# Kernel optimization log

Measured on AMD Instinct MI355X. Metric: run time of the kernel, lower is better.

## Reference

```python
import jax, jax.numpy as jnp
import numpy as np

B, S, D, H = 4, 2048, 1024, 16
HD = D // H
BITS = 8
LEVELS = 2 ** BITS - 1          # number of negative log2 levels
SCALING = 32.0 / 16.0           # lora alpha / rank for 8-bit adapter
NEG_INF = -1e9


def log_fake_quant(x, reduce_axes):
    """Per-channel log-domain fake quantization with straight-through estimator.
    Scale = per-channel max-abs; magnitudes snapped to power-of-two fractions of scale."""
    s = jnp.maximum(jnp.max(jnp.abs(x), axis=reduce_axes, keepdims=True), 1e-8)
    ratio = jnp.clip(jnp.abs(x) / s, 2.0 ** (-LEVELS), 1.0)
    e = jnp.round(jnp.log2(ratio))                      # in [-LEVELS, 0]
    q = jnp.sign(x) * s * jnp.exp2(e)
    return x + jax.lax.stop_gradient(q - x)             # STE


def cpt_linear(x, W, b, lA, lB):
    """CPTLinear: fake-quantized activation/weight GEMM + bias + LoRA on the fp input."""
    xq = log_fake_quant(x, tuple(range(x.ndim - 1)))     # per last-dim channel
    Wq = log_fake_quant(W, (1,))                         # per output row (channel_dim=0)
    out = xq @ Wq.T + b
    return out + (x @ lA @ lB) * SCALING


def setup_inputs() -> dict:
    key = jax.random.key(0)
    ks = jax.random.split(key, 8)
    causal = jnp.tril(jnp.ones((S, S), dtype=bool))
    mask = jnp.where(causal, 0.0, NEG_INF).astype(jnp.float32)[None, None]  # [1,1,S,S]
    return {
        "hidden_states": jax.random.normal(ks[0], (B, S, D), jnp.float32),
        "attention_mask": mask,
        "W_attn": jax.random.normal(ks[1], (3 * D, D), jnp.float32) * 0.02,
        "b_attn": jnp.zeros((3 * D,), jnp.float32),
        "lA_attn": jax.random.normal(ks[2], (D, 16), jnp.float32) * 0.01,
        "lB_attn": jax.random.normal(ks[3], (16, 3 * D), jnp.float32) * 0.01,
        "W_proj": jax.random.normal(ks[4], (D, D), jnp.float32) * 0.02,
        "b_proj": jnp.zeros((D,), jnp.float32),
        "lA_proj": jax.random.normal(ks[5], (D, 16), jnp.float32) * 0.01,
        "lB_proj": jax.random.normal(ks[6], (16, D), jnp.float32) * 0.01,
    }


def reference(hidden_states, attention_mask, W_attn, b_attn, lA_attn, lB_attn,
              W_proj, b_proj, lA_proj, lB_proj):
    qkv = cpt_linear(hidden_states, W_attn, b_attn, lA_attn, lB_attn)  # [B,S,3D]
    q, k, v = jnp.split(qkv, 3, axis=-1)

    def to_heads(t):
        return t.reshape(B, S, H, HD).transpose(0, 2, 1, 3)            # [B,H,S,HD]

    q, k, v = to_heads(q), to_heads(k), to_heads(v)
    scores = jnp.einsum("bhqd,bhkd->bhqk", q, k) / np.float32(np.sqrt(HD))
    scores = scores + attention_mask
    attn = jax.nn.softmax(scores, axis=-1)                             # dropout: eval mode (identity)
    out = jnp.einsum("bhqk,bhkd->bhqd", attn, v)
    out = out.transpose(0, 2, 1, 3).reshape(B, S, D)
    return cpt_linear(out, W_proj, b_proj, lA_proj, lB_proj)
```

## Files before the change

kernel.cpp:

```cpp
#include <hip/hip_runtime.h>

#define SS 2048
#define DD 1024
#define DQKV 3072
#define KP 1088
#define NT (KP / 32)
#define MTOT 8192
#define QKSZ ((size_t)MTOT * DD)

typedef unsigned short us;
typedef __attribute__((ext_vector_type(8))) short bf16x8;
typedef __attribute__((ext_vector_type(4))) float f32x4;
typedef __attribute__((ext_vector_type(4))) unsigned u32x4;

#define WAITVM(N) asm volatile("s_waitcnt vmcnt(" #N ")" ::: "memory")

__device__ __forceinline__ us f2bf(float f) {
    unsigned u = __float_as_uint(f);
    return (us)((u + 0x7fffu + ((u >> 16) & 1u)) >> 16);
}
__device__ __forceinline__ float bf2f(us h) { return __uint_as_float(((unsigned)h) << 16); }
__device__ __forceinline__ void split2(float q, us& h, us& l) {
    h = f2bf(q); l = f2bf(q - bf2f(h));
}
__device__ __forceinline__ unsigned cvtpk(float lo, float hi) {
    unsigned r;
    asm("v_cvt_pk_bf16_f32 %0, %1, %2" : "=v"(r) : "v"(lo), "v"(hi));
    return r;
}

__device__ __forceinline__ int logq_e(float ax, float s) {
    int e = 0;
    if (ax < s) {
        double r = (double)ax / (double)s;
        int ex;
        double mant = frexp(r, &ex);
        e = (mant >= 0.70710678118654752440) ? ex : ex - 1;
        e = (e < -255) ? -255 : e;
    }
    return e;
}
__device__ __forceinline__ float logq_exact(float x, float s) {
    float ax = fabsf(x);
    if (ax == 0.f) return copysignf(0.f, x);
    return copysignf(ldexpf(s, logq_e(ax, s)), x);
}

__device__ __forceinline__ void gll16(const void* g, void* l) {
    __builtin_amdgcn_global_load_lds(
        (const __attribute__((address_space(1))) void*)g,
        (__attribute__((address_space(3))) void*)l, 16, 0, 0);
}


__global__ void k_zero(unsigned* p, int n) {
    int i = blockIdx.x * 256 + threadIdx.x;
    if (i < n) p[i] = 0u;
}

__global__ void k_colmax(const float* __restrict__ x, unsigned* __restrict__ smax) {
    int c = blockIdx.x * 256 + threadIdx.x;
    int r0 = blockIdx.y * 128;
    float m = 0.f;
    for (int r = 0; r < 128; ++r) m = fmaxf(m, fabsf(x[(size_t)(r0 + r) * DD + c]));
    atomicMax(smax + c, __float_as_uint(m));
}

__global__ void k_quant_rows(const float* __restrict__ x, const unsigned* __restrict__ smax,
                             us* __restrict__ xq) {
    int m = blockIdx.x, tx = threadIdx.x;
    float4 xv = ((const float4*)(x + (size_t)m * DD))[tx];
    int c = tx * 4;
    float vv[4] = {xv.x, xv.y, xv.z, xv.w};
    ushort4 qh;
    us* ph = (us*)&qh;
#pragma unroll
    for (int j = 0; j < 4; ++j) {
        float s = fmaxf(__uint_as_float(smax[c + j]), 1e-8f);
        float sh = bf2f(f2bf(s));
        float ax = fabsf(vv[j]);
        if (ax == 0.f) ph[j] = (us)((__float_as_uint(vv[j]) >> 16) & 0x8000u);
        else ph[j] = f2bf(copysignf(ldexpf(sh, logq_e(ax, s)), vv[j]));
    }
    *(ushort4*)(xq + (size_t)m * KP + c) = qh;
    if (tx == 0) xq[(size_t)m * KP + 1056] = 0x3F80;
    else if (tx < 32) xq[(size_t)m * KP + 1056 + tx] = 0;
}

__global__ void k_lora_x(const float* __restrict__ x, const float* __restrict__ lA,
                         us* __restrict__ xq) {
    int w = threadIdx.x >> 6, lane = threadIdx.x & 63;
    int m = blockIdx.x * 4 + w;
    const float* xr = x + (size_t)m * DD;
    float acc[16];
#pragma unroll
    for (int r = 0; r < 16; ++r) acc[r] = 0.f;
#pragma unroll
    for (int i = 0; i < 4; ++i) {
        int c0 = i * 256 + lane * 4;
        float4 xv = *(const float4*)(xr + c0);
        float xs4[4] = {xv.x, xv.y, xv.z, xv.w};
#pragma unroll
        for (int j = 0; j < 4; ++j) {
            float xs = xs4[j];
            const float4* lr = (const float4*)(lA + (size_t)(c0 + j) * 16);
            float4 a0 = lr[0], a1 = lr[1], a2 = lr[2], a3 = lr[3];
            acc[0] += xs * a0.x; acc[1] += xs * a0.y; acc[2] += xs * a0.z; acc[3] += xs * a0.w;
            acc[4] += xs * a1.x; acc[5] += xs * a1.y; acc[6] += xs * a1.z; acc[7] += xs * a1.w;
            acc[8] += xs * a2.x; acc[9] += xs * a2.y; acc[10] += xs * a2.z; acc[11] += xs * a2.w;
            acc[12] += xs * a3.x; acc[13] += xs * a3.y; acc[14] += xs * a3.z; acc[15] += xs * a3.w;
        }
    }
#pragma unroll
    for (int msk = 1; msk < 64; msk <<= 1)
#pragma unroll
        for (int r = 0; r < 16; ++r) acc[r] += __shfl_xor(acc[r], msk);
    if (lane == 0) {
#pragma unroll
        for (int r = 0; r < 16; ++r) {
            us h, l; split2(2.0f * acc[r], h, l);
            xq[(size_t)m * KP + 1024 + r] = h;
            xq[(size_t)m * KP + 1040 + r] = l;
        }
    }
}

__global__ __launch_bounds__(256) void k_quant_w(const float* __restrict__ W, const float* __restrict__ lB,
                                                 const float* __restrict__ bias,
                                                 const unsigned* __restrict__ smax,
                                                 us* __restrict__ wh, us* __restrict__ wl, int Nn) {
    __shared__ float red[4];
    int n = blockIdx.x, tx = threadIdx.x;
    int lane = tx & 63, w = tx >> 6;
    float4 wv = ((const float4*)(W + (size_t)n * DD))[tx];
    float m4 = fmaxf(fmaxf(fabsf(wv.x), fabsf(wv.y)), fmaxf(fabsf(wv.z), fabsf(wv.w)));
#pragma unroll
    for (int msk = 1; msk < 64; msk <<= 1) m4 = fmaxf(m4, __shfl_xor(m4, msk));
    if (lane == 0) red[w] = m4;
    __syncthreads();
    float t = fmaxf(fmaxf(fmaxf(red[0], red[1]), fmaxf(red[2], red[3])), 1e-8f);
    float vv[4] = {wv.x, wv.y, wv.z, wv.w};
    int c = tx * 4;
    ushort4 qh, ql;
    us* ph = (us*)&qh; us* pl = (us*)&ql;
#pragma unroll
    for (int j = 0; j < 4; ++j) {
        float s = fmaxf(__uint_as_float(smax[c + j]), 1e-8f);
        float sh = bf2f(f2bf(s));
        float rho = (s - sh) / sh;
        float q = logq_exact(vv[j], t);
        float wp = q + q * rho;
        split2(wp, ph[j], pl[j]);
    }
    *(ushort4*)(wh + (size_t)n * KP + c) = qh;
    *(ushort4*)(wl + (size_t)n * KP + c) = ql;
    if (tx < 64) {
        us h = 0, l = 0;
        if (tx < 32) { int r = tx & 15; split2(lB[(size_t)r * Nn + n], h, l); }
        else if (tx == 32) split2(bias[n], h, l);
        wh[(size_t)n * KP + 1024 + tx] = h;
        wl[(size_t)n * KP + 1024 + tx] = l;
    }
}


template <int MODE>
__global__ __launch_bounds__(256) void k_gemm(const us* __restrict__ Aq_,
                                              const us* __restrict__ Bh_, const us* __restrict__ Bl_,
                                              float* __restrict__ C, int Nn,
                                              us* __restrict__ Khg, us* __restrict__ Klg,
                                              float* __restrict__ vbuf) {
    __shared__ us LA[2][4096], LBh[2][4096], LBl[2][4096];
    int tid = threadIdx.x;
    int bm = blockIdx.x, bn = blockIdx.y;
    int lane = tid & 63, w = tid >> 6;
    int wm = w >> 1, wn = w & 1;
    int l15 = lane & 15, l4 = lane >> 4;
    int gsrc = ((tid & 3) ^ ((tid >> 3) & 3)) * 8;
    const us* aP  = Aq_ + (size_t)(bm * 128 + (tid >> 2)) * KP + gsrc;
    const us* bhP = Bh_ + (size_t)(bn * 128 + (tid >> 2)) * KP + gsrc;
    const us* blP = Bl_ + (size_t)(bn * 128 + (tid >> 2)) * KP + gsrc;
    f32x4 zero4 = {0.f, 0.f, 0.f, 0.f};
    f32x4 acc[4][4];
#pragma unroll
    for (int i = 0; i < 4; ++i)
#pragma unroll
        for (int j = 0; j < 4; ++j) acc[i][j] = zero4;

#define GSTAGE(buf, kt)                                            \
    do {                                                           \
        int k0_ = (kt) * 32;                                       \
        gll16(aP + k0_,  &LA[(buf)][0] + tid * 8);                 \
        gll16(aP + (size_t)64 * KP + k0_,  &LA[(buf)][2048] + tid * 8);  \
        gll16(bhP + k0_, &LBh[(buf)][0] + tid * 8);                \
        gll16(bhP + (size_t)64 * KP + k0_, &LBh[(buf)][2048] + tid * 8); \
        gll16(blP + k0_, &LBl[(buf)][0] + tid * 8);                \
        gll16(blP + (size_t)64 * KP + k0_, &LBl[(buf)][2048] + tid * 8); \
    } while (0)

    GSTAGE(0, 0);
    GSTAGE(1, 1);
    int cur = 0;
    int gsw = (l4 ^ ((l15 >> 1) & 3)) * 8;
    for (int kt = 0; kt < NT; ++kt) {
        if (kt + 1 < NT) WAITVM(6); else WAITVM(0);
        __builtin_amdgcn_s_barrier();
        bf16x8 ah[4], bh[4], bl[4];
#pragma unroll
        for (int i = 0; i < 4; ++i) {
            int ro = (wm * 64 + i * 16 + l15) * 32 + gsw;
            int co = (wn * 64 + i * 16 + l15) * 32 + gsw;
            ah[i] = *(const bf16x8*)(&LA[cur][0] + ro);
            bh[i] = *(const bf16x8*)(&LBh[cur][0] + co);
            bl[i] = *(const bf16x8*)(&LBl[cur][0] + co);
        }
#pragma unroll
        for (int mi = 0; mi < 4; ++mi)
#pragma unroll
            for (int ni = 0; ni < 4; ++ni) {
                acc[mi][ni] = __builtin_amdgcn_mfma_f32_16x16x32_bf16(ah[mi], bh[ni], acc[mi][ni], 0, 0, 0);
                acc[mi][ni] = __builtin_amdgcn_mfma_f32_16x16x32_bf16(ah[mi], bl[ni], acc[mi][ni], 0, 0, 0);
            }
        __builtin_amdgcn_s_barrier();
        if (kt + 2 < NT) GSTAGE(cur, kt + 2);
        cur ^= 1;
    }
#undef GSTAGE

    int plane = bn >> 3;
#pragma unroll
    for (int mi = 0; mi < 4; ++mi) {
#pragma unroll
        for (int ni = 0; ni < 4; ++ni) {
            int ncol = bn * 128 + wn * 64 + ni * 16 + l15;
            size_t mbase = (size_t)bm * 128 + wm * 64 + mi * 16 + l4 * 4;
#pragma unroll
            for (int rr = 0; rr < 4; ++rr) {
                float v = acc[mi][ni][rr];
                size_t m = mbase + rr;
                if (MODE == 0) {
                    C[m * (size_t)Nn + ncol] = v;
                } else {
                    int cc = ncol & 1023;
                    if (plane == 0) {
                        C[m * DD + cc] = v;
                    } else if (plane == 2) {
                        vbuf[m * DD + cc] = v;
                    } else {
                        us hh, ll; split2(v, hh, ll);
                        size_t d = ((size_t)((m >> 11) * 16 + (cc >> 6)) * SS + (m & 2047)) * 64 + (cc & 63);
                        Khg[d] = hh; Klg[d] = ll;
                    }
                }
            }
        }
    }
}


__global__ __launch_bounds__(256) void k_transpose_v(const float* __restrict__ vbuf,
                                                     us* __restrict__ vth, us* __restrict__ vtl) {
    __shared__ us th[64][72], tl[64][72];
    int st = blockIdx.x, bh = blockIdx.y;
    int bb = bh >> 4, h = bh & 15;
    int s0 = st * 64, tid = threadIdx.x;
    int sl = tid >> 2, c0 = (tid & 3) * 16;
    const float* src = vbuf + (size_t)(bb * SS + s0 + sl) * DD + h * 64 + c0;
#pragma unroll
    for (int j4 = 0; j4 < 4; ++j4) {
        float4 v = *(const float4*)(src + j4 * 4);
        float vv[4] = {v.x, v.y, v.z, v.w};
#pragma unroll
        for (int j = 0; j < 4; ++j) {
            us hh, ll; split2(vv[j], hh, ll);
            th[c0 + j4 * 4 + j][sl] = hh;
            tl[c0 + j4 * 4 + j][sl] = ll;
        }
    }
    __syncthreads();
#pragma unroll
    for (int p = 0; p < 2; ++p) {
        int gidx = p * 256 + tid;
        int hd = gidx >> 3, g = gidx & 7;
        int base = (g >> 2) * 32 + (g & 3) * 4;
        ushort4 a, b2, c, d2;
        a.x = th[hd][base];      a.y = th[hd][base + 1];  a.z = th[hd][base + 2];  a.w = th[hd][base + 3];
        b2.x = th[hd][base + 16]; b2.y = th[hd][base + 17]; b2.z = th[hd][base + 18]; b2.w = th[hd][base + 19];
        c.x = tl[hd][base];      c.y = tl[hd][base + 1];  c.z = tl[hd][base + 2];  c.w = tl[hd][base + 3];
        d2.x = tl[hd][base + 16]; d2.y = tl[hd][base + 17]; d2.z = tl[hd][base + 18]; d2.w = tl[hd][base + 19];
        size_t dof = ((size_t)bh * 64 + hd) * SS + s0 + g * 8;
        *(ushort4*)(vth + dof) = a;  *(ushort4*)(vth + dof + 4) = b2;
        *(ushort4*)(vtl + dof) = c;  *(ushort4*)(vtl + dof + 4) = d2;
    }
}


#define SCL 0.18033688011112042f

__global__ __launch_bounds__(256, 2) void k_attn(float* qo,
                                                 const us* __restrict__ Khg, const us* __restrict__ Klg,
                                                 const us* __restrict__ vth, const us* __restrict__ vtl) {
    __shared__ us L[2][16384];
    int bh = blockIdx.x;
    int qt = (int)(gridDim.y - 1) - blockIdx.y;
    int b = bh >> 4, h = bh & 15;
    int q0 = qt * 128;
    int tid = threadIdx.x, w = tid >> 6, lane = tid & 63;
    int l15 = lane & 15, l4 = lane >> 4;
    int qw = q0 + w * 32;
    int swz = l15 & 7;

    bf16x8 qh[2][2], ql[2][2];
#pragma unroll
    for (int qb = 0; qb < 2; ++qb)
#pragma unroll
        for (int hf = 0; hf < 2; ++hf) {
            const float* qp = qo + (size_t)(b * SS + qw + qb * 16 + l15) * DD + h * 64 + hf * 32 + l4 * 8;
            float4 a = *(const float4*)qp;
            float4 c = *(const float4*)(qp + 4);
            float vv[8] = {a.x, a.y, a.z, a.w, c.x, c.y, c.z, c.w};
            bf16x8 hq, lq;
#pragma unroll
            for (int j = 0; j < 8; ++j) {
                us hh = f2bf(vv[j]);
                hq[j] = (short)hh;
                lq[j] = (short)f2bf(vv[j] - bf2f(hh));
            }
            qh[qb][hf] = hq; ql[qb][hf] = lq;
        }

    f32x4 zero4 = {0.f, 0.f, 0.f, 0.f};
    f32x4 of[2][4];
#pragma unroll
    for (int i = 0; i < 2; ++i)
#pragma unroll
        for (int j = 0; j < 4; ++j) of[i][j] = zero4;
    float mrow[2] = {-1e30f, -1e30f}, lrow[2] = {0.f, 0.f};

    int r0 = tid >> 3, sl0 = (tid & 7) ^ (r0 & 7);
    int g1 = tid + 256, r1 = g1 >> 3, sl1 = (g1 & 7) ^ (r1 & 7);
    int koff0 = (bh * SS + r0) * 64 + sl0 * 8;
    int koff1 = (bh * SS + r1) * 64 + sl1 * 8;
    int voff0 = (bh * 64 + r0) * SS + sl0 * 8;
    int voff1 = (bh * 64 + r1) * SS + sl1 * 8;

    int ntiles = qt * 2 + 2;

#define STAGE(buf, tt)                                           \
    do {                                                         \
        int kv_ = (tt) * 64;                                     \
        us* D_ = &L[(buf)][0];                                   \
        int kadd_ = kv_ << 6;                                    \
        gll16(Khg + koff0 + kadd_, D_ + tid * 8);                \
        gll16(Khg + koff1 + kadd_, D_ + 2048 + tid * 8);         \
        gll16(Klg + koff0 + kadd_, D_ + 4096 + tid * 8);         \
        gll16(Klg + koff1 + kadd_, D_ + 6144 + tid * 8);         \
        gll16(vth + voff0 + kv_, D_ + 8192 + tid * 8);           \
        gll16(vth + voff1 + kv_, D_ + 10240 + tid * 8);          \
        gll16(vtl + voff0 + kv_, D_ + 12288 + tid * 8);          \
        gll16(vtl + voff1 + kv_, D_ + 14336 + tid * 8);          \
    } while (0)

    STAGE(0, 0);
    STAGE(1, 1);
    int cur = 0;

    for (int t = 0; t < ntiles; ++t) {
        int kv0 = t * 64;
        if (t + 1 < ntiles) WAITVM(8); else WAITVM(0);
        __builtin_amdgcn_s_barrier();

        if (kv0 <= qw + 31) {
            const us* Lc = &L[cur][0];

            f32x4 sf[4][2];
#pragma unroll
            for (int i = 0; i < 4; ++i) { sf[i][0] = zero4; sf[i][1] = zero4; }
            __builtin_amdgcn_s_setprio(1);
#pragma unroll
            for (int kb = 0; kb < 4; ++kb) {
                int rbase = (kb * 16 + l15) * 64;
#pragma unroll
                for (int hf = 0; hf < 2; ++hf) {
                    int off = rbase + (((hf * 4 + l4) ^ swz) * 8);
                    bf16x8 kh = *(const bf16x8*)(Lc + off);
                    bf16x8 kl = *(const bf16x8*)(Lc + 4096 + off);
#pragma unroll
                    for (int qb = 0; qb < 2; ++qb) {
                        sf[kb][qb] = __builtin_amdgcn_mfma_f32_16x16x32_bf16(kh, qh[qb][hf], sf[kb][qb], 0, 0, 0);
                        sf[kb][qb] = __builtin_amdgcn_mfma_f32_16x16x32_bf16(kh, ql[qb][hf], sf[kb][qb], 0, 0, 0);
                        sf[kb][qb] = __builtin_amdgcn_mfma_f32_16x16x32_bf16(kl, qh[qb][hf], sf[kb][qb], 0, 0, 0);
                    }
                }
            }
            __builtin_amdgcn_s_setprio(0);

            bool diag = (kv0 + 63 > qw);
            u32x4 PH[2][2], PL[2][2];
#pragma unroll
            for (int qb = 0; qb < 2; ++qb) {
                float pv[16];
                if (diag) {
                    int qg = qw + qb * 16 + l15;
#pragma unroll
                    for (int kb = 0; kb < 4; ++kb)
#pragma unroll
                        for (int rr = 0; rr < 4; ++rr) {
                            int kvg = kv0 + kb * 16 + l4 * 4 + rr;
                            float sc = sf[kb][qb][rr] * SCL;
                            pv[kb * 4 + rr] = (kvg > qg) ? -1e30f : sc;
                        }
                } else {
#pragma unroll
                    for (int kb = 0; kb < 4; ++kb)
#pragma unroll
                        for (int rr = 0; rr < 4; ++rr)
                            pv[kb * 4 + rr] = sf[kb][qb][rr] * SCL;
                }
                float tmax = pv[0];
#pragma unroll
                for (int i = 1; i < 16; ++i) tmax = fmaxf(tmax, pv[i]);
                tmax = fmaxf(tmax, __shfl_xor(tmax, 16));
                tmax = fmaxf(tmax, __shfl_xor(tmax, 32));
                float mnew = fmaxf(mrow[qb], tmax);
                float fac = __builtin_amdgcn_exp2f(mrow[qb] - mnew);
                mrow[qb] = mnew;
                float ps = 0.f;
#pragma unroll
                for (int i = 0; i < 16; ++i) {
                    pv[i] = __builtin_amdgcn_exp2f(pv[i] - mnew);
                    ps += pv[i];
                }
                ps += __shfl_xor(ps, 16); ps += __shfl_xor(ps, 32);
                lrow[qb] = lrow[qb] * fac + ps;
#pragma unroll
                for (int ks = 0; ks < 2; ++ks)
#pragma unroll
                    for (int c2 = 0; c2 < 4; ++c2) {
                        float p0 = pv[ks * 8 + c2 * 2], p1 = pv[ks * 8 + c2 * 2 + 1];
                        unsigned u = cvtpk(p0, p1);
                        float h0 = __uint_as_float(u << 16);
                        float h1 = __uint_as_float(u & 0xffff0000u);
                        unsigned ul = cvtpk(p0 - h0, p1 - h1);
                        PH[qb][ks][c2] = u; PL[qb][ks][c2] = ul;
                    }
                float fr0 = __shfl(fac, l4 * 4 + 0);
                float fr1 = __shfl(fac, l4 * 4 + 1);
                float fr2 = __shfl(fac, l4 * 4 + 2);
                float fr3 = __shfl(fac, l4 * 4 + 3);
#pragma unroll
                for (int hb = 0; hb < 4; ++hb) {
                    of[qb][hb][0] *= fr0; of[qb][hb][1] *= fr1;
                    of[qb][hb][2] *= fr2; of[qb][hb][3] *= fr3;
                }
            }

            __builtin_amdgcn_s_setprio(1);
#pragma unroll
            for (int hb = 0; hb < 4; ++hb) {
                int rbase = (hb * 16 + l15) * 64;
#pragma unroll
                for (int ks = 0; ks < 2; ++ks) {
                    int off = rbase + (((ks * 4 + l4) ^ swz) * 8);
                    bf16x8 vh = *(const bf16x8*)(Lc + 8192 + off);
                    bf16x8 vl = *(const bf16x8*)(Lc + 12288 + off);
#pragma unroll
                    for (int qb = 0; qb < 2; ++qb) {
                        bf16x8 pa = (bf16x8)PH[qb][ks];
                        bf16x8 pb = (bf16x8)PL[qb][ks];
                        of[qb][hb] = __builtin_amdgcn_mfma_f32_16x16x32_bf16(pa, vh, of[qb][hb], 0, 0, 0);
                        of[qb][hb] = __builtin_amdgcn_mfma_f32_16x16x32_bf16(pa, vl, of[qb][hb], 0, 0, 0);
                        of[qb][hb] = __builtin_amdgcn_mfma_f32_16x16x32_bf16(pb, vh, of[qb][hb], 0, 0, 0);
                    }
                }
            }
            __builtin_amdgcn_s_setprio(0);
        }

        __builtin_amdgcn_s_barrier();
        if (t + 2 < ntiles) STAGE(cur, t + 2);
        cur ^= 1;
    }
#undef STAGE

#pragma unroll
    for (int qb = 0; qb < 2; ++qb) {
        float linv = 1.f / lrow[qb];
        float f0 = __shfl(linv, l4 * 4 + 0);
        float f1 = __shfl(linv, l4 * 4 + 1);
        float f2 = __shfl(linv, l4 * 4 + 2);
        float f3 = __shfl(linv, l4 * 4 + 3);
        int qgb = qw + qb * 16 + l4 * 4;
#pragma unroll
        for (int hb = 0; hb < 4; ++hb) {
            int col = h * 64 + hb * 16 + l15;
            qo[((size_t)(b * SS + qgb + 0)) * DD + col] = of[qb][hb][0] * f0;
            qo[((size_t)(b * SS + qgb + 1)) * DD + col] = of[qb][hb][1] * f1;
            qo[((size_t)(b * SS + qgb + 2)) * DD + col] = of[qb][hb][2] * f2;
            qo[((size_t)(b * SS + qgb + 3)) * DD + col] = of[qb][hb][3] * f3;
        }
    }
}


extern "C" void kernel_launch(void* const* d_in, const int* in_sizes, int n_in,
                              void* d_out, int out_size, void* d_ws, size_t ws_size,
                              hipStream_t stream) {
    const float* hidden  = (const float*)d_in[0];
    const float* W_attn  = (const float*)d_in[2];
    const float* b_attn  = (const float*)d_in[3];
    const float* lA_attn = (const float*)d_in[4];
    const float* lB_attn = (const float*)d_in[5];
    const float* W_proj  = (const float*)d_in[6];
    const float* b_proj  = (const float*)d_in[7];
    const float* lA_proj = (const float*)d_in[8];
    const float* lB_proj = (const float*)d_in[9];
    float* out = (float*)d_out;

    char* ws = (char*)d_ws;
    unsigned* s1 = (unsigned*)(ws);
    unsigned* s2 = (unsigned*)(ws + 4096);
    us* xq  = (us*)(ws + 8192);
    us* vth = xq;
    us* wh1 = (us*)(ws + 8192 + 17825792);
    us* wl1 = (us*)(ws + 8192 + 17825792 + 6684672);
    us* wh2 = (us*)(ws + 8192 + 17825792 + 2 * 6684672);
    us* wl2 = (us*)(ws + 8192 + 17825792 + 2 * 6684672 + 2228224);
    char* pbase = ws + 8192 + 17825792 + 2 * 6684672 + 2 * 2228224;
    float* qbuf = (float*)pbase;
    float* vbuf = (float*)(pbase + 33554432);
    us* Khg = (us*)(pbase + 2 * (size_t)33554432);
    us* Klg = (us*)(pbase + 2 * (size_t)33554432 + 16777216);
    us* vtl = (us*)(pbase + 2 * (size_t)33554432 + 2 * (size_t)16777216);

    k_zero<<<8, 256, 0, stream>>>(s1, 2048);

    k_colmax<<<dim3(4, 64), 256, 0, stream>>>(hidden, s1);
    k_quant_rows<<<MTOT, 256, 0, stream>>>(hidden, s1, xq);
    k_lora_x<<<MTOT / 4, 256, 0, stream>>>(hidden, lA_attn, xq);
    k_quant_w<<<3072, 256, 0, stream>>>(W_attn, lB_attn, b_attn, s1, wh1, wl1, 3072);
    k_gemm<1><<<dim3(64, 24), 256, 0, stream>>>(xq, wh1, wl1, qbuf, DQKV, Khg, Klg, vbuf);

    k_transpose_v<<<dim3(32, 64), 256, 0, stream>>>(vbuf, vth, vtl);
    k_attn<<<dim3(64, 16), 256, 0, stream>>>(qbuf, Khg, Klg, vth, vtl);

    k_colmax<<<dim3(4, 64), 256, 0, stream>>>(qbuf, s2);
    k_quant_rows<<<MTOT, 256, 0, stream>>>(qbuf, s2, xq);
    k_lora_x<<<MTOT / 4, 256, 0, stream>>>(qbuf, lA_proj, xq);
    k_quant_w<<<1024, 256, 0, stream>>>(W_proj, lB_proj, b_proj, s2, wh2, wl2, 1024);
    k_gemm<0><<<dim3(64, 8), 256, 0, stream>>>(xq, wh2, wl2, out, DD, nullptr, nullptr, nullptr);
}
```

Baseline: 499.0 us.

## Enlarge GEMM tile to 256x128 with 512 threads and 64-wide K steps

Restructures the split-bf16 GEMM so each block computes a 256x128 output tile with 8 waves and stages 64-wide K slices, changing the LDS swizzle to match. The K step is split into two halves, with the next stage's global loads issued between them, and s_setprio raises priority around the MFMA bursts. The aim is more operand reuse per LDS byte, fewer K-loop iterations and barriers, and better overlap of loads with MFMA. In exchange, LDS use doubles (128 KB per block) and register pressure rises, which may limit occupancy; the launch grids shrink to match.

Measured after the change: 473.1 us. 5.2% less time.

```diff
diff --git a/kernel.cpp b/kernel.cpp
--- a/kernel.cpp
+++ b/kernel.cpp
@@ -4,7 +4,7 @@
 #define DD 1024
 #define DQKV 3072
 #define KP 1088
-#define NT (KP / 32)
+#define NT64 17
 #define MTOT 8192
 #define QKSZ ((size_t)MTOT * DD)
 
@@ -14,6 +14,7 @@
 typedef __attribute__((ext_vector_type(4))) unsigned u32x4;
 
 #define WAITVM(N) asm volatile("s_waitcnt vmcnt(" #N ")" ::: "memory")
+#define WAITLGKM0 asm volatile("s_waitcnt lgkmcnt(0)" ::: "memory")
 
 __device__ __forceinline__ us f2bf(float f) {
     unsigned u = __float_as_uint(f);
@@ -165,75 +166,110 @@
 
 
 template <int MODE>
-__global__ __launch_bounds__(256) void k_gemm(const us* __restrict__ Aq_,
-                                              const us* __restrict__ Bh_, const us* __restrict__ Bl_,
-                                              float* __restrict__ C, int Nn,
-                                              us* __restrict__ Khg, us* __restrict__ Klg,
-                                              float* __restrict__ vbuf) {
-    __shared__ us LA[2][4096], LBh[2][4096], LBl[2][4096];
+__global__ __launch_bounds__(512, 2) void k_gemm(const us* __restrict__ Aq_,
+                                                 const us* __restrict__ Bh_, const us* __restrict__ Bl_,
+                                                 float* __restrict__ C, int Nn,
+                                                 us* __restrict__ Khg, us* __restrict__ Klg,
+                                                 float* __restrict__ vbuf) {
+    __shared__ us LA[2][16384];
+    __shared__ us LBh[2][8192];
+    __shared__ us LBl[2][8192];
     int tid = threadIdx.x;
     int bm = blockIdx.x, bn = blockIdx.y;
     int lane = tid & 63, w = tid >> 6;
-    int wm = w >> 1, wn = w & 1;
+    int wm = w >> 2, wn = w & 3;
     int l15 = lane & 15, l4 = lane >> 4;
-    int gsrc = ((tid & 3) ^ ((tid >> 3) & 3)) * 8;
-    const us* aP  = Aq_ + (size_t)(bm * 128 + (tid >> 2)) * KP + gsrc;
-    const us* bhP = Bh_ + (size_t)(bn * 128 + (tid >> 2)) * KP + gsrc;
-    const us* blP = Bl_ + (size_t)(bn * 128 + (tid >> 2)) * KP + gsrc;
+    int srow = tid >> 3;
+    int gsrc = ((tid & 7) ^ (srow & 7)) * 8;
+    const us* aP  = Aq_ + (size_t)(bm * 256 + srow) * KP + gsrc;
+    const us* bhP = Bh_ + (size_t)(bn * 128 + srow) * KP + gsrc;
+    const us* blP = Bl_ + (size_t)(bn * 128 + srow) * KP + gsrc;
     f32x4 zero4 = {0.f, 0.f, 0.f, 0.f};
-    f32x4 acc[4][4];
-#pragma unroll
-    for (int i = 0; i < 4; ++i)
-#pragma unroll
-        for (int j = 0; j < 4; ++j) acc[i][j] = zero4;
-
-#define GSTAGE(buf, kt)                                            \
-    do {                                                           \
-        int k0_ = (kt) * 32;                                       \
-        gll16(aP + k0_,  &LA[(buf)][0] + tid * 8);                 \
-        gll16(aP + (size_t)64 * KP + k0_,  &LA[(buf)][2048] + tid * 8);  \
-        gll16(bhP + k0_, &LBh[(buf)][0] + tid * 8);                \
-        gll16(bhP + (size_t)64 * KP + k0_, &LBh[(buf)][2048] + tid * 8); \
-        gll16(blP + k0_, &LBl[(buf)][0] + tid * 8);                \
-        gll16(blP + (size_t)64 * KP + k0_, &LBl[(buf)][2048] + tid * 8); \
+    f32x4 acc[8][2];
+#pragma unroll
+    for (int i = 0; i < 8; ++i) { acc[i][0] = zero4; acc[i][1] = zero4; }
+
+#define GSTAGE(buf, kt)                                               \
+    do {                                                              \
+        int k0_ = (kt) * 64;                                          \
+        gll16(aP + k0_,                    &LA[(buf)][0]     + tid * 8); \
+        gll16(aP + (size_t)64  * KP + k0_, &LA[(buf)][4096]  + tid * 8); \
+        gll16(aP + (size_t)128 * KP + k0_, &LA[(buf)][8192]  + tid * 8); \
+        gll16(aP + (size_t)192 * KP + k0_, &LA[(buf)][12288] + tid * 8); \
+        gll16(bhP + k0_,                   &LBh[(buf)][0]    + tid * 8); \
+        gll16(bhP + (size_t)64 * KP + k0_, &LBh[(buf)][4096] + tid * 8); \
+        gll16(blP + k0_,                   &LBl[(buf)][0]    + tid * 8); \
+        gll16(blP + (size_t)64 * KP + k0_, &LBl[(buf)][4096] + tid * 8); \
     } while (0)
 
     GSTAGE(0, 0);
     GSTAGE(1, 1);
+    WAITVM(8);
+    __builtin_amdgcn_s_barrier();
+    __builtin_amdgcn_sched_barrier(0);
+
+    int gsw0 = ((l4)     ^ (l15 & 7)) * 8;
+    int gsw1 = ((4 + l4) ^ (l15 & 7)) * 8;
     int cur = 0;
-    int gsw = (l4 ^ ((l15 >> 1) & 3)) * 8;
-    for (int kt = 0; kt < NT; ++kt) {
-        if (kt + 1 < NT) WAITVM(6); else WAITVM(0);
+    for (int kt = 0; kt < NT64; ++kt) {
+        const us* A0  = &LA[cur][0];
+        const us* Bh0 = &LBh[cur][0];
+        const us* Bl0 = &LBl[cur][0];
+        bf16x8 a0[8], b0h[2], b0l[2];
+#pragma unroll
+        for (int i = 0; i < 8; ++i)
+            a0[i] = *(const bf16x8*)(A0 + (wm * 128 + i * 16 + l15) * 64 + gsw0);
+#pragma unroll
+        for (int i = 0; i < 2; ++i) {
+            b0h[i] = *(const bf16x8*)(Bh0 + (wn * 32 + i * 16 + l15) * 64 + gsw0);
+            b0l[i] = *(const bf16x8*)(Bl0 + (wn * 32 + i * 16 + l15) * 64 + gsw0);
+        }
+        __builtin_amdgcn_s_setprio(1);
+#pragma unroll
+        for (int mi = 0; mi < 8; ++mi)
+#pragma unroll
+            for (int ni = 0; ni < 2; ++ni) {
+                acc[mi][ni] = __builtin_amdgcn_mfma_f32_16x16x32_bf16(a0[mi], b0h[ni], acc[mi][ni], 0, 0, 0);
+                acc[mi][ni] = __builtin_amdgcn_mfma_f32_16x16x32_bf16(a0[mi], b0l[ni], acc[mi][ni], 0, 0, 0);
+            }
+        __builtin_amdgcn_s_setprio(0);
+        bf16x8 a1[8], b1h[2], b1l[2];
+#pragma unroll
+        for (int i = 0; i < 8; ++i)
+            a1[i] = *(const bf16x8*)(A0 + (wm * 128 + i * 16 + l15) * 64 + gsw1);
+#pragma unroll
+        for (int i = 0; i < 2; ++i) {
+            b1h[i] = *(const bf16x8*)(Bh0 + (wn * 32 + i * 16 + l15) * 64 + gsw1);
+            b1l[i] = *(const bf16x8*)(Bl0 + (wn * 32 + i * 16 + l15) * 64 + gsw1);
+        }
+        WAITLGKM0;
+        __builtin_amdgcn_sched_barrier(0);
         __builtin_amdgcn_s_barrier();
-        bf16x8 ah[4], bh[4], bl[4];
-#pragma unroll
-        for (int i = 0; i < 4; ++i) {
-            int ro = (wm * 64 + i * 16 + l15) * 32 + gsw;
-            int co = (wn * 64 + i * 16 + l15) * 32 + gsw;
-            ah[i] = *(const bf16x8*)(&LA[cur][0] + ro);
-            bh[i] = *(const bf16x8*)(&LBh[cur][0] + co);
-            bl[i] = *(const bf16x8*)(&LBl[cur][0] + co);
-        }
-#pragma unroll
-        for (int mi = 0; mi < 4; ++mi)
-#pragma unroll
-            for (int ni = 0; ni < 4; ++ni) {
-                acc[mi][ni] = __builtin_amdgcn_mfma_f32_16x16x32_bf16(ah[mi], bh[ni], acc[mi][ni], 0, 0, 0);
-                acc[mi][ni] = __builtin_amdgcn_mfma_f32_16x16x32_bf16(ah[mi], bl[ni], acc[mi][ni], 0, 0, 0);
-            }
+        __builtin_amdgcn_sched_barrier(0);
+        if (kt + 2 < NT64) GSTAGE(cur, kt + 2);
+        __builtin_amdgcn_s_setprio(1);
+#pragma unroll
+        for (int mi = 0; mi < 8; ++mi)
+#pragma unroll
+            for (int ni = 0; ni < 2; ++ni) {
+                acc[mi][ni] = __builtin_amdgcn_mfma_f32_16x16x32_bf16(a1[mi], b1h[ni], acc[mi][ni], 0, 0, 0);
+                acc[mi][ni] = __builtin_amdgcn_mfma_f32_16x16x32_bf16(a1[mi], b1l[ni], acc[mi][ni], 0, 0, 0);
+            }
+        __builtin_amdgcn_s_setprio(0);
+        if (kt + 2 < NT64) { WAITVM(8); } else { WAITVM(0); }
         __builtin_amdgcn_s_barrier();
-        if (kt + 2 < NT) GSTAGE(cur, kt + 2);
+        __builtin_amdgcn_sched_barrier(0);
         cur ^= 1;
     }
 #undef GSTAGE
 
     int plane = bn >> 3;
 #pragma unroll
-    for (int mi = 0; mi < 4; ++mi) {
-#pragma unroll
-        for (int ni = 0; ni < 4; ++ni) {
-            int ncol = bn * 128 + wn * 64 + ni * 16 + l15;
-            size_t mbase = (size_t)bm * 128 + wm * 64 + mi * 16 + l4 * 4;
+    for (int mi = 0; mi < 8; ++mi) {
+#pragma unroll
+        for (int ni = 0; ni < 2; ++ni) {
+            int ncol = bn * 128 + wn * 32 + ni * 16 + l15;
+            size_t mbase = (size_t)bm * 256 + wm * 128 + mi * 16 + l4 * 4;
 #pragma unroll
             for (int rr = 0; rr < 4; ++rr) {
                 float v = acc[mi][ni][rr];
@@ -539,7 +575,7 @@
     k_quant_rows<<<MTOT, 256, 0, stream>>>(hidden, s1, xq);
     k_lora_x<<<MTOT / 4, 256, 0, stream>>>(hidden, lA_attn, xq);
     k_quant_w<<<3072, 256, 0, stream>>>(W_attn, lB_attn, b_attn, s1, wh1, wl1, 3072);
-    k_gemm<1><<<dim3(64, 24), 256, 0, stream>>>(xq, wh1, wl1, qbuf, DQKV, Khg, Klg, vbuf);
+    k_gemm<1><<<dim3(32, 24), 512, 0, stream>>>(xq, wh1, wl1, qbuf, DQKV, Khg, Klg, vbuf);
 
     k_transpose_v<<<dim3(32, 64), 256, 0, stream>>>(vbuf, vth, vtl);
     k_attn<<<dim3(64, 16), 256, 0, stream>>>(qbuf, Khg, Klg, vth, vtl);
@@ -548,5 +584,5 @@
     k_quant_rows<<<MTOT, 256, 0, stream>>>(qbuf, s2, xq);
     k_lora_x<<<MTOT / 4, 256, 0, stream>>>(qbuf, lA_proj, xq);
     k_quant_w<<<1024, 256, 0, stream>>>(W_proj, lB_proj, b_proj, s2, wh2, wl2, 1024);
-    k_gemm<0><<<dim3(64, 8), 256, 0, stream>>>(xq, wh2, wl2, out, DD, nullptr, nullptr, nullptr);
-}
+    k_gemm<0><<<dim3(32, 8), 512, 0, stream>>>(xq, wh2, wl2, out, DD, nullptr, nullptr, nullptr);
+}
```
